# Optimization experiments

Hardware: AMD Instinct MI355X
Metric: run time of the kernel (lower is better)

The kernel has to match this reference:

```python
import jax, jax.numpy as jnp
import numpy as np

N, D_IN, H, C, K = 16384, 2048, 4096, 256, 256


def setup_inputs() -> dict:
    key = jax.random.key(0)
    ks = jax.random.split(key, 13)

    def lin(kw, kb, fan_in, fan_out):
        # torch Linear default init: U(-1/sqrt(fan_in), 1/sqrt(fan_in)); stored as [in, out]
        bound = 1.0 / np.sqrt(fan_in)
        W = jax.random.uniform(kw, (fan_in, fan_out), jnp.float32, -bound, bound)
        b = jax.random.uniform(kb, (fan_out,), jnp.float32, -bound, bound)
        return W, b

    W_e1, b_e1 = lin(ks[0], ks[1], D_IN, H)
    W_e2, b_e2 = lin(ks[2], ks[3], H, C)
    W_d1, b_d1 = lin(ks[4], ks[5], C, H)
    W_d2, b_d2 = lin(ks[6], ks[7], H, D_IN)
    # codebooks init U(-1/K, 1/K) per the torch code
    cb1 = jax.random.uniform(ks[8], (K, C), jnp.float32, -1.0 / K, 1.0 / K)
    cb2 = jax.random.uniform(ks[9], (K, C), jnp.float32, -1.0 / K, 1.0 / K)
    cb3 = jax.random.uniform(ks[10], (K, C), jnp.float32, -1.0 / K, 1.0 / K)
    x = jax.random.normal(ks[11], (N, D_IN), jnp.float32)
    return {"x": x, "W_e1": W_e1, "b_e1": b_e1, "W_e2": W_e2, "b_e2": b_e2,
            "cb1": cb1, "cb2": cb2, "cb3": cb3,
            "W_d1": W_d1, "b_d1": b_d1, "W_d2": W_d2, "b_d2": b_d2}


def _vq_stage(z, cb):
    # dist[n,k] = sum_c (cb[k,c] - z[n,c])^2 = ||z||^2 - 2 z.cb^T + ||cb||^2
    # (same math as the torch N x K x C broadcast, expressed as a GEMM)
    d = (jnp.sum(z * z, axis=1, keepdims=True)
         - 2.0 * (z @ cb.T)
         + jnp.sum(cb * cb, axis=1))            # [N, K]
    nearest = jnp.argmin(d, axis=1)             # [N]
    zq = cb[nearest]                            # gather [N, C]
    return nearest, zq


def reference(x, W_e1, b_e1, W_e2, b_e2, cb1, cb2, cb3, W_d1, b_d1, W_d2, b_d2):
    ze_1 = jax.nn.relu(x @ W_e1 + b_e1) @ W_e2 + b_e2     # [N, C]
    nearest_1, zq_1 = _vq_stage(ze_1, cb1)
    ze_2 = ze_1 - zq_1
    nearest_2, zq_2 = _vq_stage(ze_2, cb2)
    ze_3 = ze_2 - zq_2
    nearest_3, zq_3 = _vq_stage(ze_3, cb3)
    # straight-through estimator
    decoder_input = ze_1 + jax.lax.stop_gradient(zq_1 + zq_2 + zq_3 - ze_1)
    x_hat = jax.nn.sigmoid(decoder_input @ W_d1 + b_d1) @ W_d2 + b_d2
    return (x_hat, ze_1, ze_2, ze_3, zq_1, zq_2, zq_3, nearest_1, nearest_2, nearest_3)
```

## Files before the change

kernel.cpp:

```cpp
#include <hip/hip_runtime.h>
#include <cstddef>


#define NN 16384
#define DIN 2048
#define HH 4096
#define CC 256

typedef __attribute__((ext_vector_type(8))) short bf16x8;
typedef __attribute__((ext_vector_type(4))) float f32x4;

__device__ inline unsigned short f2b(float v) {
    unsigned int u = __float_as_uint(v);
    return (unsigned short)((u + 0x7fffu + ((u >> 16) & 1u)) >> 16);
}
__device__ inline float b2f(unsigned short s) {
    return __uint_as_float(((unsigned int)s) << 16);
}

template<int NP>
__launch_bounds__(256)
__global__ void tsplit(const float* __restrict__ W,
                       unsigned short* __restrict__ T0,
                       unsigned short* __restrict__ T1,
                       unsigned short* __restrict__ T2,
                       int K, int N)
{
    __shared__ float tile[32][33];
    const int k0 = blockIdx.y * 32, n0 = blockIdx.x * 32;
    const int c = threadIdx.x & 31, r = threadIdx.x >> 5;
    #pragma unroll
    for (int i = 0; i < 4; ++i)
        tile[r + 8*i][c] = W[(size_t)(k0 + r + 8*i) * N + n0 + c];
    __syncthreads();
    #pragma unroll
    for (int i = 0; i < 4; ++i) {
        const int nl = r + 8*i, kl = c;
        float v = tile[kl][nl];
        size_t o = (size_t)(n0 + nl) * K + k0 + kl;
        unsigned short h = f2b(v);
        T0[o] = h;
        if (NP > 1) {
            float r1 = v - b2f(h);
            unsigned short m = f2b(r1);
            T1[o] = m;
            T2[o] = f2b(r1 - b2f(m));
        }
    }
}

template<int NP, int EPI>
__launch_bounds__(256)
__global__ void gemm_sp(const float* __restrict__ A,
                        const unsigned short* __restrict__ B0,
                        const unsigned short* __restrict__ B1,
                        const unsigned short* __restrict__ B2,
                        const float* __restrict__ bias,
                        float* __restrict__ Cf,
                        int M, int N, int K)
{
    __shared__ unsigned short As[NP][128][32];
    __shared__ unsigned short Bs[NP][128][32];

    const int t    = threadIdx.x;
    const int wid  = t >> 6;
    const int lane = t & 63;
    const int bm   = blockIdx.y * 128;
    const int bn   = blockIdx.x * 128;
    const int wm   = (wid >> 1) * 64;
    const int wn   = (wid & 1) * 64;
    const int l15  = lane & 15;
    const int l4   = lane >> 4;

    f32x4 acc[4][4] = {};

    const unsigned short* Bp[3] = {B0, B1, B2};

    for (int k0 = 0; k0 < K; k0 += 32) {
        float4 av[4];
        #pragma unroll
        for (int i = 0; i < 4; ++i) {
            const int chunk = t + i * 256;
            const int arow  = chunk >> 3;
            const int ac4   = (chunk & 7) << 2;
            av[i] = *(const float4*)(A + (size_t)(bm + arow) * K + k0 + ac4);
        }
        bf16x8 bv[NP][2];
        #pragma unroll
        for (int p = 0; p < NP; ++p)
            #pragma unroll
            for (int i = 0; i < 2; ++i) {
                const int chunk = t + i * 256;
                const int brow  = chunk >> 2;
                const int bc8   = (chunk & 3) << 3;
                bv[p][i] = *(const bf16x8*)(Bp[p] + (size_t)(bn + brow) * K + k0 + bc8);
            }

        __syncthreads();

        #pragma unroll
        for (int i = 0; i < 4; ++i) {
            const int chunk = t + i * 256;
            const int arow  = chunk >> 3;
            const int ac4   = (chunk & 7) << 2;
            float vs[4] = {av[i].x, av[i].y, av[i].z, av[i].w};
            ushort4 hv, mv, lv;
            unsigned short* hp = (unsigned short*)&hv;
            unsigned short* mp = (unsigned short*)&mv;
            unsigned short* lp = (unsigned short*)&lv;
            #pragma unroll
            for (int j = 0; j < 4; ++j) {
                float v = vs[j];
                unsigned short h = f2b(v);
                hp[j] = h;
                if (NP > 1) {
                    float r1 = v - b2f(h);
                    unsigned short m = f2b(r1);
                    mp[j] = m;
                    lp[j] = f2b(r1 - b2f(m));
                }
            }
            *(ushort4*)&As[0][arow][ac4] = hv;
            if (NP > 1) {
                *(ushort4*)&As[1][arow][ac4] = mv;
                *(ushort4*)&As[2][arow][ac4] = lv;
            }
        }
        #pragma unroll
        for (int p = 0; p < NP; ++p)
            #pragma unroll
            for (int i = 0; i < 2; ++i) {
                const int chunk = t + i * 256;
                const int brow  = chunk >> 2;
                const int bc8   = (chunk & 3) << 3;
                *(bf16x8*)&Bs[p][brow][bc8] = bv[p][i];
            }

        __syncthreads();

        const int nprod = (NP == 3) ? 6 : 1;
        const int pa[6] = {0, 0, 1, 0, 1, 2};
        const int pb[6] = {0, 1, 0, 2, 1, 0};
        #pragma unroll
        for (int q = 0; q < 6; ++q) {
            if (q >= nprod) break;
            const int ia = pa[q], ib = pb[q];
            bf16x8 af[4], bfr[4];
            #pragma unroll
            for (int mi = 0; mi < 4; ++mi)
                af[mi] = *(const bf16x8*)&As[ia][wm + mi*16 + l15][l4 * 8];
            #pragma unroll
            for (int ni = 0; ni < 4; ++ni)
                bfr[ni] = *(const bf16x8*)&Bs[ib][wn + ni*16 + l15][l4 * 8];
            #pragma unroll
            for (int mi = 0; mi < 4; ++mi)
                #pragma unroll
                for (int ni = 0; ni < 4; ++ni)
                    acc[mi][ni] = __builtin_amdgcn_mfma_f32_16x16x32_bf16(
                        af[mi], bfr[ni], acc[mi][ni], 0, 0, 0);
        }
    }

    #pragma unroll
    for (int ni = 0; ni < 4; ++ni) {
        const int gcol = bn + wn + ni*16 + l15;
        const float bvv = bias[gcol];
        #pragma unroll
        for (int mi = 0; mi < 4; ++mi) {
            #pragma unroll
            for (int r = 0; r < 4; ++r) {
                float v = acc[mi][ni][r] + bvv;
                if (EPI == 1) v = fmaxf(v, 0.0f);
                if (EPI == 2) v = 1.0f / (1.0f + expf(-v));
                const int grow = bm + wm + mi*16 + l4*4 + r;
                Cf[(size_t)grow * N + gcol] = v;
            }
        }
    }
}

template<int EPI>
__launch_bounds__(256)
__global__ void gemm_f32(const float* __restrict__ A, const float* __restrict__ B,
                         const float* __restrict__ bias, float* __restrict__ C,
                         int M, int N, int K)
{
    __shared__ float As[16][132];
    __shared__ float Bs[16][132];
    const int t  = threadIdx.x;
    const int tx = t & 15;
    const int ty = t >> 4;
    const int bm = blockIdx.y * 128;
    const int bn = blockIdx.x * 128;
    const int ar  = t >> 2;
    const int ac  = (t & 3) << 2;
    const int bkr = t >> 5;
    const int bc  = (t & 31) << 2;
    const float* Ap0 = A + (size_t)(bm + ar)      * K + ac;
    const float* Ap1 = A + (size_t)(bm + ar + 64) * K + ac;
    const float* Bp0 = B + (size_t)bkr       * N + bn + bc;
    const float* Bp1 = B + (size_t)(bkr + 8) * N + bn + bc;
    float acc[8][8] = {};
    for (int k0 = 0; k0 < K; k0 += 16) {
        float4 a0 = *(const float4*)(Ap0 + k0);
        float4 a1 = *(const float4*)(Ap1 + k0);
        float4 b0 = *(const float4*)(Bp0 + (size_t)k0 * N);
        float4 b1 = *(const float4*)(Bp1 + (size_t)k0 * N);
        __syncthreads();
        As[ac+0][ar] = a0.x; As[ac+1][ar] = a0.y;
        As[ac+2][ar] = a0.z; As[ac+3][ar] = a0.w;
        As[ac+0][ar+64] = a1.x; As[ac+1][ar+64] = a1.y;
        As[ac+2][ar+64] = a1.z; As[ac+3][ar+64] = a1.w;
        *(float4*)&Bs[bkr][bc]   = b0;
        *(float4*)&Bs[bkr+8][bc] = b1;
        __syncthreads();
        #pragma unroll
        for (int k = 0; k < 16; ++k) {
            float4 xa0 = *(const float4*)&As[k][ty*8];
            float4 xa1 = *(const float4*)&As[k][ty*8+4];
            float4 xb0 = *(const float4*)&Bs[k][tx*8];
            float4 xb1 = *(const float4*)&Bs[k][tx*8+4];
            float avr[8] = {xa0.x,xa0.y,xa0.z,xa0.w,xa1.x,xa1.y,xa1.z,xa1.w};
            float bvr[8] = {xb0.x,xb0.y,xb0.z,xb0.w,xb1.x,xb1.y,xb1.z,xb1.w};
            #pragma unroll
            for (int i = 0; i < 8; ++i)
                #pragma unroll
                for (int j = 0; j < 8; ++j)
                    acc[i][j] = fmaf(avr[i], bvr[j], acc[i][j]);
        }
    }
    float4 bb0 = *(const float4*)(bias + bn + tx*8);
    float4 bb1 = *(const float4*)(bias + bn + tx*8 + 4);
    float bcol[8] = {bb0.x,bb0.y,bb0.z,bb0.w,bb1.x,bb1.y,bb1.z,bb1.w};
    #pragma unroll
    for (int i = 0; i < 8; ++i) {
        const int row = bm + ty*8 + i;
        float o[8];
        #pragma unroll
        for (int j = 0; j < 8; ++j) {
            float v = acc[i][j] + bcol[j];
            if (EPI == 1) v = fmaxf(v, 0.0f);
            if (EPI == 2) v = 1.0f / (1.0f + expf(-v));
            o[j] = v;
        }
        float4 o0 = {o[0],o[1],o[2],o[3]};
        float4 o1 = {o[4],o[5],o[6],o[7]};
        float* cp = C + (size_t)row * N + bn + tx*8;
        *(float4*)cp       = o0;
        *(float4*)(cp + 4) = o1;
    }
}

__launch_bounds__(256)
__global__ void vq_kernel(const float* __restrict__ ze1,
                          const float* __restrict__ cb1,
                          const float* __restrict__ cb2,
                          const float* __restrict__ cb3,
                          float* __restrict__ out_ze2, float* __restrict__ out_ze3,
                          float* __restrict__ out_zq1, float* __restrict__ out_zq2,
                          float* __restrict__ out_zq3,
                          float* __restrict__ out_n1,  float* __restrict__ out_n2,
                          float* __restrict__ out_n3,
                          float* __restrict__ dec_in)
{
    __shared__ float Zs[16][260];
    __shared__ float Ds[16][260];
    __shared__ float DecS[16][260];
    __shared__ float Srow[16];
    __shared__ int   Kmin[16];

    const int t    = threadIdx.x;
    const int row0 = blockIdx.x * 16;

    for (int i = t; i < 16*64; i += 256) {
        int r = i >> 6, c4 = (i & 63) << 2;
        float4 v = *(const float4*)(ze1 + (size_t)(row0 + r) * 256 + c4);
        *(float4*)&Zs[r][c4] = v;
        float4 z = {0.f,0.f,0.f,0.f};
        *(float4*)&DecS[r][c4] = z;
    }
    __syncthreads();

    const float* cbs[3] = {cb1, cb2, cb3};
    float* zqs[3] = {out_zq1, out_zq2, out_zq3};
    float* nss[3] = {out_n1, out_n2, out_n3};

    for (int s = 0; s < 3; ++s) {
        const float* cb = cbs[s];
        if (t < 16) {
            float ssum = 0.f;
            for (int c = 0; c < 256; ++c) ssum = fmaf(Zs[t][c], Zs[t][c], ssum);
            Srow[t] = ssum;
        }
        __syncthreads();
        {
            float accr[16];
            #pragma unroll
            for (int r = 0; r < 16; ++r) accr[r] = 0.f;
            float c2 = 0.f;
            const float* cbrow = cb + (size_t)t * 256;
            for (int c4 = 0; c4 < 256; c4 += 4) {
                float4 cv = *(const float4*)(cbrow + c4);
                c2 = fmaf(cv.x,cv.x,fmaf(cv.y,cv.y,fmaf(cv.z,cv.z,fmaf(cv.w,cv.w,c2))));
                #pragma unroll
                for (int r = 0; r < 16; ++r) {
                    float4 zv = *(const float4*)&Zs[r][c4];
                    accr[r] = fmaf(zv.x,cv.x,fmaf(zv.y,cv.y,
                              fmaf(zv.z,cv.z,fmaf(zv.w,cv.w,accr[r]))));
                }
            }
            #pragma unroll
            for (int r = 0; r < 16; ++r) {
                float g2 = __fmul_rn(2.0f, accr[r]);
                float t1 = __fsub_rn(Srow[r], g2);
                Ds[r][t]  = __fadd_rn(t1, c2);
            }
        }
        __syncthreads();
        if (t < 16) {
            float best = Ds[t][0];
            int bk = 0;
            for (int k = 1; k < 256; ++k) {
                float v = Ds[t][k];
                if (v < best) { best = v; bk = k; }
            }
            Kmin[t] = bk;
            nss[s][row0 + t] = (float)bk;
        }
        __syncthreads();
        for (int i = t; i < 16*64; i += 256) {
            int r = i >> 6, c4 = (i & 63) << 2;
            const float* q = cb + (size_t)Kmin[r] * 256 + c4;
            float4 qv = *(const float4*)q;
            *(float4*)&zqs[s][(size_t)(row0 + r) * 256 + c4] = qv;
            float4 dv = *(float4*)&DecS[r][c4];
            dv.x = __fadd_rn(dv.x, qv.x); dv.y = __fadd_rn(dv.y, qv.y);
            dv.z = __fadd_rn(dv.z, qv.z); dv.w = __fadd_rn(dv.w, qv.w);
            *(float4*)&DecS[r][c4] = dv;
            if (s < 2) {
                float4 zv = *(float4*)&Zs[r][c4];
                zv.x = __fsub_rn(zv.x, qv.x); zv.y = __fsub_rn(zv.y, qv.y);
                zv.z = __fsub_rn(zv.z, qv.z); zv.w = __fsub_rn(zv.w, qv.w);
                *(float4*)&Zs[r][c4] = zv;
                float* oz = (s == 0) ? out_ze2 : out_ze3;
                *(float4*)&oz[(size_t)(row0 + r) * 256 + c4] = zv;
            }
        }
        __syncthreads();
    }

    for (int i = t; i < 16*64; i += 256) {
        int r = i >> 6, c4 = (i & 63) << 2;
        float4 z1 = *(const float4*)(ze1 + (size_t)(row0 + r) * 256 + c4);
        float4 dv = *(float4*)&DecS[r][c4];
        float4 o;
        o.x = __fadd_rn(z1.x, __fsub_rn(dv.x, z1.x));
        o.y = __fadd_rn(z1.y, __fsub_rn(dv.y, z1.y));
        o.z = __fadd_rn(z1.z, __fsub_rn(dv.z, z1.z));
        o.w = __fadd_rn(z1.w, __fsub_rn(dv.w, z1.w));
        *(float4*)&dec_in[(size_t)(row0 + r) * 256 + c4] = o;
    }
}

extern "C" void kernel_launch(void* const* d_in, const int* in_sizes, int n_in,
                              void* d_out, int out_size, void* d_ws, size_t ws_size,
                              hipStream_t stream)
{
    const float* x   = (const float*)d_in[0];
    const float* We1 = (const float*)d_in[1];
    const float* be1 = (const float*)d_in[2];
    const float* We2 = (const float*)d_in[3];
    const float* be2 = (const float*)d_in[4];
    const float* cb1 = (const float*)d_in[5];
    const float* cb2 = (const float*)d_in[6];
    const float* cb3 = (const float*)d_in[7];
    const float* Wd1 = (const float*)d_in[8];
    const float* bd1 = (const float*)d_in[9];
    const float* Wd2 = (const float*)d_in[10];
    const float* bd2 = (const float*)d_in[11];

    float* out   = (float*)d_out;
    float* x_hat = out;
    float* ze1   = out + 33554432;
    float* ze2   = out + 37748736;
    float* ze3   = out + 41943040;
    float* zq1   = out + 46137344;
    float* zq2   = out + 50331648;
    float* zq3   = out + 54525952;
    float* n1    = out + 58720256;
    float* n2    = out + 58736640;
    float* n3    = out + 58753024;

    float* h   = (float*)d_ws;
    float* dec = h + (size_t)NN * HH;
    unsigned short* We1t = (unsigned short*)(dec + (size_t)NN * CC);
    size_t szWe1 = (size_t)HH * DIN;
    unsigned short* We2t = We1t + 3 * szWe1;
    size_t szWe2 = (size_t)CC * HH;
    unsigned short* Wd1t = We2t + 3 * szWe2;
    size_t szWd1 = (size_t)HH * CC;
    unsigned short* Wd2t = Wd1t + szWd1;
    size_t szWd2 = (size_t)DIN * HH;
    size_t need = (size_t)((unsigned short*)(Wd2t + szWd2) - (unsigned short*)d_ws) * 2;

    dim3 blk(256);

    if (ws_size >= need) {
        tsplit<3><<<dim3(HH/32, DIN/32), blk, 0, stream>>>(We1, We1t, We1t+szWe1, We1t+2*szWe1, DIN, HH);
        tsplit<3><<<dim3(CC/32, HH/32),  blk, 0, stream>>>(We2, We2t, We2t+szWe2, We2t+2*szWe2, HH, CC);
        tsplit<1><<<dim3(HH/32, CC/32),  blk, 0, stream>>>(Wd1, Wd1t, nullptr, nullptr, CC, HH);
        tsplit<1><<<dim3(DIN/32, HH/32), blk, 0, stream>>>(Wd2, Wd2t, nullptr, nullptr, HH, DIN);

        gemm_sp<3,1><<<dim3(HH/128, NN/128), blk, 0, stream>>>(x, We1t, We1t+szWe1, We1t+2*szWe1, be1, h, NN, HH, DIN);
        gemm_sp<3,0><<<dim3(CC/128, NN/128), blk, 0, stream>>>(h, We2t, We2t+szWe2, We2t+2*szWe2, be2, ze1, NN, CC, HH);
        vq_kernel<<<dim3(NN/16), blk, 0, stream>>>(ze1, cb1, cb2, cb3,
                                                   ze2, ze3, zq1, zq2, zq3,
                                                   n1, n2, n3, dec);
        gemm_sp<1,2><<<dim3(HH/128, NN/128), blk, 0, stream>>>(dec, Wd1t, nullptr, nullptr, bd1, h, NN, HH, CC);
        gemm_sp<1,0><<<dim3(DIN/128, NN/128), blk, 0, stream>>>(h, Wd2t, nullptr, nullptr, bd2, x_hat, NN, DIN, HH);
    } else {
        float* h1  = (float*)d_ws;
        float* dcf = h1 + (size_t)NN * HH;
        gemm_f32<1><<<dim3(HH/128, NN/128), blk, 0, stream>>>(x, We1, be1, h1, NN, HH, DIN);
        gemm_f32<0><<<dim3(CC/128, NN/128), blk, 0, stream>>>(h1, We2, be2, ze1, NN, CC, HH);
        vq_kernel<<<dim3(NN/16), blk, 0, stream>>>(ze1, cb1, cb2, cb3,
                                                   ze2, ze3, zq1, zq2, zq3,
                                                   n1, n2, n3, dcf);
        gemm_f32<2><<<dim3(HH/128, NN/128), blk, 0, stream>>>(dcf, Wd1, bd1, h1, NN, HH, CC);
        gemm_f32<0><<<dim3(DIN/128, NN/128), blk, 0, stream>>>(h1, Wd2, bd2, x_hat, NN, DIN, HH);
    }
}
```

Baseline: 2.538 ms.

## Pre-split activations to bf16 planes, load tiles via global_load_lds with swizzle

Activations are now split into three bf16 planes ahead of time, either by a dedicated kernel or in the previous GEMM's epilogue, so the GEMMs stream pre-split A tiles straight into LDS with global_load_lds. The LDS layout is XOR-swizzled and workgroup IDs are remapped for L2 locality. The decoder path now stores intermediates as single bf16 instead of fp32, which halves activation traffic. The goal is to cut per-tile split arithmetic, register staging and LDS bank conflicts. The cost is much more workspace and memory writes for the 3-plane hidden activations.

```diff
diff --git a/kernel.cpp b/kernel.cpp
--- a/kernel.cpp
+++ b/kernel.cpp
@@ -7,23 +7,37 @@
 #define HH 4096
 #define CC 256
 
+typedef unsigned short ushortT;
 typedef __attribute__((ext_vector_type(8))) short bf16x8;
 typedef __attribute__((ext_vector_type(4))) float f32x4;
 
-__device__ inline unsigned short f2b(float v) {
+__device__ __forceinline__ ushortT f2b(float v) {
     unsigned int u = __float_as_uint(v);
-    return (unsigned short)((u + 0x7fffu + ((u >> 16) & 1u)) >> 16);
-}
-__device__ inline float b2f(unsigned short s) {
+    return (ushortT)((u + 0x7fffu + ((u >> 16) & 1u)) >> 16);
+}
+__device__ __forceinline__ float b2f(ushortT s) {
     return __uint_as_float(((unsigned int)s) << 16);
+}
+__device__ __forceinline__ void split3(float v, ushortT& h, ushortT& m, ushortT& l) {
+    h = f2b(v);
+    float r1 = v - b2f(h);
+    m = f2b(r1);
+    l = f2b(r1 - b2f(m));
+}
+
+__device__ __forceinline__ void gld16(const void* g, void* l) {
+    __builtin_amdgcn_global_load_lds(
+        (const __attribute__((address_space(1))) unsigned int*)g,
+        (__attribute__((address_space(3))) unsigned int*)l,
+        16, 0, 0);
 }
 
 template<int NP>
 __launch_bounds__(256)
 __global__ void tsplit(const float* __restrict__ W,
-                       unsigned short* __restrict__ T0,
-                       unsigned short* __restrict__ T1,
-                       unsigned short* __restrict__ T2,
+                       ushortT* __restrict__ T0,
+                       ushortT* __restrict__ T1,
+                       ushortT* __restrict__ T2,
                        int K, int N)
 {
     __shared__ float tile[32][33];
@@ -38,126 +52,173 @@
         const int nl = r + 8*i, kl = c;
         float v = tile[kl][nl];
         size_t o = (size_t)(n0 + nl) * K + k0 + kl;
-        unsigned short h = f2b(v);
+        ushortT h = f2b(v);
         T0[o] = h;
         if (NP > 1) {
             float r1 = v - b2f(h);
-            unsigned short m = f2b(r1);
+            ushortT m = f2b(r1);
             T1[o] = m;
             T2[o] = f2b(r1 - b2f(m));
         }
     }
 }
 
-template<int NP, int EPI>
 __launch_bounds__(256)
-__global__ void gemm_sp(const float* __restrict__ A,
-                        const unsigned short* __restrict__ B0,
-                        const unsigned short* __restrict__ B1,
-                        const unsigned short* __restrict__ B2,
+__global__ void split_src(const float* __restrict__ X,
+                          ushortT* __restrict__ P0, ushortT* __restrict__ P1,
+                          ushortT* __restrict__ P2, size_t n4)
+{
+    for (size_t i = (size_t)blockIdx.x * 256 + threadIdx.x; i < n4;
+         i += (size_t)gridDim.x * 256) {
+        float4 v = *(const float4*)(X + i * 4);
+        ushort4 hv, mv, lv;
+        split3(v.x, ((ushortT*)&hv)[0], ((ushortT*)&mv)[0], ((ushortT*)&lv)[0]);
+        split3(v.y, ((ushortT*)&hv)[1], ((ushortT*)&mv)[1], ((ushortT*)&lv)[1]);
+        split3(v.z, ((ushortT*)&hv)[2], ((ushortT*)&mv)[2], ((ushortT*)&lv)[2]);
+        split3(v.w, ((ushortT*)&hv)[3], ((ushortT*)&mv)[3], ((ushortT*)&lv)[3]);
+        *(ushort4*)(P0 + i * 4) = hv;
+        *(ushort4*)(P1 + i * 4) = mv;
+        *(ushort4*)(P2 + i * 4) = lv;
+    }
+}
+
+template<int NPA, int INA, int EPI, int OM>
+__launch_bounds__(256)
+__global__ void gemm_mp(const float* __restrict__ Af,
+                        const ushortT* __restrict__ Ap0,
+                        const ushortT* __restrict__ Ap1,
+                        const ushortT* __restrict__ Ap2,
+                        const ushortT* __restrict__ B0,
+                        const ushortT* __restrict__ B1,
+                        const ushortT* __restrict__ B2,
                         const float* __restrict__ bias,
                         float* __restrict__ Cf,
+                        ushortT* __restrict__ O0, ushortT* __restrict__ O1,
+                        ushortT* __restrict__ O2,
                         int M, int N, int K)
 {
-    __shared__ unsigned short As[NP][128][32];
-    __shared__ unsigned short Bs[NP][128][32];
+    __shared__ ushortT sh[2 * NPA * 4096];
 
     const int t    = threadIdx.x;
     const int wid  = t >> 6;
     const int lane = t & 63;
-    const int bm   = blockIdx.y * 128;
-    const int bn   = blockIdx.x * 128;
-    const int wm   = (wid >> 1) * 64;
-    const int wn   = (wid & 1) * 64;
     const int l15  = lane & 15;
     const int l4   = lane >> 4;
 
+    const int gx  = gridDim.x;
+    const int nwg = gx * gridDim.y;
+    const int lin = blockIdx.y * gx + blockIdx.x;
+    const int swz = (lin & 7) * (nwg >> 3) + (lin >> 3);
+    const int bm  = (swz / gx) * 128;
+    const int bn  = (swz % gx) * 128;
+
+    const int wm = (wid >> 1) * 64;
+    const int wn = (wid & 1) * 64;
+
+    const ushortT* APs[3] = {Ap0, Ap1, Ap2};
+    const ushortT* BPs[3] = {B0, B1, B2};
+
+    const int CHB = 2 * NPA;
+    const int CHA = (INA == 1) ? 2 * NPA : 0;
+    const ushortT* gpA[(INA == 1) ? 2 * NPA : 1];
+    const ushortT* gpB[2 * NPA];
+    if (INA == 1) {
+        #pragma unroll
+        for (int i = 0; i < CHA; ++i) {
+            int chunk = i * 256 + t;
+            int plane = chunk >> 9;
+            int c     = chunk & 511;
+            int row   = c >> 2;
+            int colsw = (c & 3) ^ ((c >> 4) & 3);
+            gpA[i] = APs[plane] + (size_t)(bm + row) * K + colsw * 8;
+        }
+    }
+    #pragma unroll
+    for (int i = 0; i < CHB; ++i) {
+        int chunk = i * 256 + t;
+        int plane = chunk >> 9;
+        int c     = chunk & 511;
+        int row   = c >> 2;
+        int colsw = (c & 3) ^ ((c >> 4) & 3);
+        gpB[i] = BPs[plane] + (size_t)(bn + row) * K + colsw * 8;
+    }
+    const int arow_ = t >> 3;
+    const int ac4_  = (t & 7) << 2;
+    const int aswc_ = ((ac4_ >> 3) ^ ((arow_ >> 2) & 3)) * 8 + (ac4_ & 7);
+
+    const int sws = (l4 ^ (l15 >> 2)) * 8;
+
     f32x4 acc[4][4] = {};
-
-    const unsigned short* Bp[3] = {B0, B1, B2};
 
     for (int k0 = 0; k0 < K; k0 += 32) {
         float4 av[4];
+        if (INA == 0) {
+            #pragma unroll
+            for (int i = 0; i < 4; ++i) {
+                const int chunk = t + i * 256;
+                const int arow  = chunk >> 3;
+                const int ac4   = (chunk & 7) << 2;
+                av[i] = *(const float4*)(Af + (size_t)(bm + arow) * K + k0 + ac4);
+            }
+        }
+
+        __syncthreads();
+
+        if (INA == 1) {
+            #pragma unroll
+            for (int i = 0; i < CHA; ++i) {
+                gld16(gpA[i], sh + ((size_t)i * 256 + t) * 8);
+                gpA[i] += 32;
+            }
+        }
         #pragma unroll
-        for (int i = 0; i < 4; ++i) {
-            const int chunk = t + i * 256;
-            const int arow  = chunk >> 3;
-            const int ac4   = (chunk & 7) << 2;
-            av[i] = *(const float4*)(A + (size_t)(bm + arow) * K + k0 + ac4);
-        }
-        bf16x8 bv[NP][2];
+        for (int i = 0; i < CHB; ++i) {
+            gld16(gpB[i], sh + (size_t)NPA * 4096 + ((size_t)i * 256 + t) * 8);
+            gpB[i] += 32;
+        }
+        if (INA == 0) {
+            #pragma unroll
+            for (int i = 0; i < 4; ++i) {
+                const int chunk = t + i * 256;
+                const int arow  = chunk >> 3;
+                const int ac4   = (chunk & 7) << 2;
+                const int swc   = ((ac4 >> 3) ^ ((arow >> 2) & 3)) * 8 + (ac4 & 7);
+                float vs[4] = {av[i].x, av[i].y, av[i].z, av[i].w};
+                ushort4 hv, mv, lv;
+                #pragma unroll
+                for (int j = 0; j < 4; ++j)
+                    split3(vs[j], ((ushortT*)&hv)[j], ((ushortT*)&mv)[j],
+                           ((ushortT*)&lv)[j]);
+                *(ushort4*)&sh[0 * 4096 + arow * 32 + swc] = hv;
+                if (NPA > 1) {
+                    *(ushort4*)&sh[1 * 4096 + arow * 32 + swc] = mv;
+                    *(ushort4*)&sh[2 * 4096 + arow * 32 + swc] = lv;
+                }
+            }
+        }
+
+        __syncthreads();
+
         #pragma unroll
-        for (int p = 0; p < NP; ++p)
-            #pragma unroll
-            for (int i = 0; i < 2; ++i) {
-                const int chunk = t + i * 256;
-                const int brow  = chunk >> 2;
-                const int bc8   = (chunk & 3) << 3;
-                bv[p][i] = *(const bf16x8*)(Bp[p] + (size_t)(bn + brow) * K + k0 + bc8);
-            }
-
-        __syncthreads();
-
-        #pragma unroll
-        for (int i = 0; i < 4; ++i) {
-            const int chunk = t + i * 256;
-            const int arow  = chunk >> 3;
-            const int ac4   = (chunk & 7) << 2;
-            float vs[4] = {av[i].x, av[i].y, av[i].z, av[i].w};
-            ushort4 hv, mv, lv;
-            unsigned short* hp = (unsigned short*)&hv;
-            unsigned short* mp = (unsigned short*)&mv;
-            unsigned short* lp = (unsigned short*)&lv;
-            #pragma unroll
-            for (int j = 0; j < 4; ++j) {
-                float v = vs[j];
-                unsigned short h = f2b(v);
-                hp[j] = h;
-                if (NP > 1) {
-                    float r1 = v - b2f(h);
-                    unsigned short m = f2b(r1);
-                    mp[j] = m;
-                    lp[j] = f2b(r1 - b2f(m));
-                }
-            }
-            *(ushort4*)&As[0][arow][ac4] = hv;
-            if (NP > 1) {
-                *(ushort4*)&As[1][arow][ac4] = mv;
-                *(ushort4*)&As[2][arow][ac4] = lv;
-            }
-        }
-        #pragma unroll
-        for (int p = 0; p < NP; ++p)
-            #pragma unroll
-            for (int i = 0; i < 2; ++i) {
-                const int chunk = t + i * 256;
-                const int brow  = chunk >> 2;
-                const int bc8   = (chunk & 3) << 3;
-                *(bf16x8*)&Bs[p][brow][bc8] = bv[p][i];
-            }
-
-        __syncthreads();
-
-        const int nprod = (NP == 3) ? 6 : 1;
-        const int pa[6] = {0, 0, 1, 0, 1, 2};
-        const int pb[6] = {0, 1, 0, 2, 1, 0};
-        #pragma unroll
-        for (int q = 0; q < 6; ++q) {
-            if (q >= nprod) break;
-            const int ia = pa[q], ib = pb[q];
-            bf16x8 af[4], bfr[4];
+        for (int pa = 0; pa < NPA; ++pa) {
+            bf16x8 af[4];
             #pragma unroll
             for (int mi = 0; mi < 4; ++mi)
-                af[mi] = *(const bf16x8*)&As[ia][wm + mi*16 + l15][l4 * 8];
-            #pragma unroll
-            for (int ni = 0; ni < 4; ++ni)
-                bfr[ni] = *(const bf16x8*)&Bs[ib][wn + ni*16 + l15][l4 * 8];
-            #pragma unroll
-            for (int mi = 0; mi < 4; ++mi)
+                af[mi] = *(const bf16x8*)&sh[pa * 4096 + (wm + mi*16 + l15) * 32 + sws];
+            #pragma unroll
+            for (int pb = 0; pb < NPA - pa; ++pb) {
+                bf16x8 bfr[4];
                 #pragma unroll
                 for (int ni = 0; ni < 4; ++ni)
-                    acc[mi][ni] = __builtin_amdgcn_mfma_f32_16x16x32_bf16(
-                        af[mi], bfr[ni], acc[mi][ni], 0, 0, 0);
+                    bfr[ni] = *(const bf16x8*)&sh[(NPA + pb) * 4096 +
+                                                  (wn + ni*16 + l15) * 32 + sws];
+                #pragma unroll
+                for (int mi = 0; mi < 4; ++mi)
+                    #pragma unroll
+                    for (int ni = 0; ni < 4; ++ni)
+                        acc[mi][ni] = __builtin_amdgcn_mfma_f32_16x16x32_bf16(
+                            af[mi], bfr[ni], acc[mi][ni], 0, 0, 0);
+            }
         }
     }
 
@@ -173,81 +234,18 @@
                 if (EPI == 1) v = fmaxf(v, 0.0f);
                 if (EPI == 2) v = 1.0f / (1.0f + expf(-v));
                 const int grow = bm + wm + mi*16 + l4*4 + r;
-                Cf[(size_t)grow * N + gcol] = v;
-            }
-        }
-    }
-}
-
-template<int EPI>
-__launch_bounds__(256)
-__global__ void gemm_f32(const float* __restrict__ A, const float* __restrict__ B,
-                         const float* __restrict__ bias, float* __restrict__ C,
-                         int M, int N, int K)
-{
-    __shared__ float As[16][132];
-    __shared__ float Bs[16][132];
-    const int t  = threadIdx.x;
-    const int tx = t & 15;
-    const int ty = t >> 4;
-    const int bm = blockIdx.y * 128;
-    const int bn = blockIdx.x * 128;
-    const int ar  = t >> 2;
-    const int ac  = (t & 3) << 2;
-    const int bkr = t >> 5;
-    const int bc  = (t & 31) << 2;
-    const float* Ap0 = A + (size_t)(bm + ar)      * K + ac;
-    const float* Ap1 = A + (size_t)(bm + ar + 64) * K + ac;
-    const float* Bp0 = B + (size_t)bkr       * N + bn + bc;
-    const float* Bp1 = B + (size_t)(bkr + 8) * N + bn + bc;
-    float acc[8][8] = {};
-    for (int k0 = 0; k0 < K; k0 += 16) {
-        float4 a0 = *(const float4*)(Ap0 + k0);
-        float4 a1 = *(const float4*)(Ap1 + k0);
-        float4 b0 = *(const float4*)(Bp0 + (size_t)k0 * N);
-        float4 b1 = *(const float4*)(Bp1 + (size_t)k0 * N);
-        __syncthreads();
-        As[ac+0][ar] = a0.x; As[ac+1][ar] = a0.y;
-        As[ac+2][ar] = a0.z; As[ac+3][ar] = a0.w;
-        As[ac+0][ar+64] = a1.x; As[ac+1][ar+64] = a1.y;
-        As[ac+2][ar+64] = a1.z; As[ac+3][ar+64] = a1.w;
-        *(float4*)&Bs[bkr][bc]   = b0;
-        *(float4*)&Bs[bkr+8][bc] = b1;
-        __syncthreads();
-        #pragma unroll
-        for (int k = 0; k < 16; ++k) {
-            float4 xa0 = *(const float4*)&As[k][ty*8];
-            float4 xa1 = *(const float4*)&As[k][ty*8+4];
-            float4 xb0 = *(const float4*)&Bs[k][tx*8];
-            float4 xb1 = *(const float4*)&Bs[k][tx*8+4];
-            float avr[8] = {xa0.x,xa0.y,xa0.z,xa0.w,xa1.x,xa1.y,xa1.z,xa1.w};
-            float bvr[8] = {xb0.x,xb0.y,xb0.z,xb0.w,xb1.x,xb1.y,xb1.z,xb1.w};
-            #pragma unroll
-            for (int i = 0; i < 8; ++i)
-                #pragma unroll
-                for (int j = 0; j < 8; ++j)
-                    acc[i][j] = fmaf(avr[i], bvr[j], acc[i][j]);
-        }
-    }
-    float4 bb0 = *(const float4*)(bias + bn + tx*8);
-    float4 bb1 = *(const float4*)(bias + bn + tx*8 + 4);
-    float bcol[8] = {bb0.x,bb0.y,bb0.z,bb0.w,bb1.x,bb1.y,bb1.z,bb1.w};
-    #pragma unroll
-    for (int i = 0; i < 8; ++i) {
-        const int row = bm + ty*8 + i;
-        float o[8];
-        #pragma unroll
-        for (int j = 0; j < 8; ++j) {
-            float v = acc[i][j] + bcol[j];
-            if (EPI == 1) v = fmaxf(v, 0.0f);
-            if (EPI == 2) v = 1.0f / (1.0f + expf(-v));
-            o[j] = v;
-        }
-        float4 o0 = {o[0],o[1],o[2],o[3]};
-        float4 o1 = {o[4],o[5],o[6],o[7]};
-        float* cp = C + (size_t)row * N + bn + tx*8;
-        *(float4*)cp       = o0;
-        *(float4*)(cp + 4) = o1;
+                const size_t o = (size_t)grow * N + gcol;
+                if (OM == 0) {
+                    Cf[o] = v;
+                } else if (OM == 2) {
+                    O0[o] = f2b(v);
+                } else {
+                    ushortT hh, mm, ll;
+                    split3(v, hh, mm, ll);
+                    O0[o] = hh; O1[o] = mm; O2[o] = ll;
+                }
+            }
+        }
     }
 }
 
@@ -261,7 +259,7 @@
                           float* __restrict__ out_zq3,
                           float* __restrict__ out_n1,  float* __restrict__ out_n2,
                           float* __restrict__ out_n3,
-                          float* __restrict__ dec_in)
+                          ushortT* __restrict__ dec_p)
 {
     __shared__ float Zs[16][260];
     __shared__ float Ds[16][260];
@@ -358,7 +356,12 @@
         o.y = __fadd_rn(z1.y, __fsub_rn(dv.y, z1.y));
         o.z = __fadd_rn(z1.z, __fsub_rn(dv.z, z1.z));
         o.w = __fadd_rn(z1.w, __fsub_rn(dv.w, z1.w));
-        *(float4*)&dec_in[(size_t)(row0 + r) * 256 + c4] = o;
+        ushort4 ov;
+        ((ushortT*)&ov)[0] = f2b(o.x);
+        ((ushortT*)&ov)[1] = f2b(o.y);
+        ((ushortT*)&ov)[2] = f2b(o.z);
+        ((ushortT*)&ov)[3] = f2b(o.w);
+        *(ushort4*)(dec_p + (size_t)(row0 + r) * 256 + c4) = ov;
     }
 }
 
@@ -391,42 +394,79 @@
     float* n2    = out + 58736640;
     float* n3    = out + 58753024;
 
-    float* h   = (float*)d_ws;
-    float* dec = h + (size_t)NN * HH;
-    unsigned short* We1t = (unsigned short*)(dec + (size_t)NN * CC);
-    size_t szWe1 = (size_t)HH * DIN;
-    unsigned short* We2t = We1t + 3 * szWe1;
-    size_t szWe2 = (size_t)CC * HH;
-    unsigned short* Wd1t = We2t + 3 * szWe2;
-    size_t szWd1 = (size_t)HH * CC;
-    unsigned short* Wd2t = Wd1t + szWd1;
-    size_t szWd2 = (size_t)DIN * HH;
-    size_t need = (size_t)((unsigned short*)(Wd2t + szWd2) - (unsigned short*)d_ws) * 2;
+    const size_t szX  = (size_t)NN * DIN;
+    const size_t szH  = (size_t)NN * HH;
+    const size_t szD  = (size_t)NN * CC;
+    const size_t szW1 = (size_t)HH * DIN;
+    const size_t szW2 = (size_t)CC * HH;
+
+    const size_t needA = (3*szX + 3*szH + 3*szW1 + 3*szW2 + szW2 + szW1) * 2;
 
     dim3 blk(256);
 
-    if (ws_size >= need) {
-        tsplit<3><<<dim3(HH/32, DIN/32), blk, 0, stream>>>(We1, We1t, We1t+szWe1, We1t+2*szWe1, DIN, HH);
-        tsplit<3><<<dim3(CC/32, HH/32),  blk, 0, stream>>>(We2, We2t, We2t+szWe2, We2t+2*szWe2, HH, CC);
+    if (ws_size >= needA) {
+        ushortT* xp0 = (ushortT*)d_ws;
+        ushortT* xp1 = xp0 + szX;
+        ushortT* xp2 = xp1 + szX;
+        ushortT* hp0 = xp2 + szX;
+        ushortT* hp1 = hp0 + szH;
+        ushortT* hp2 = hp1 + szH;
+        ushortT* We1t = hp2 + szH;
+        ushortT* We2t = We1t + 3*szW1;
+        ushortT* Wd1t = We2t + 3*szW2;
+        ushortT* Wd2t = Wd1t + szW2;
+        ushortT* decp = xp0;
+        ushortT* h2p  = xp0 + szD;
+
+        tsplit<3><<<dim3(HH/32, DIN/32), blk, 0, stream>>>(We1, We1t, We1t+szW1, We1t+2*szW1, DIN, HH);
+        tsplit<3><<<dim3(CC/32, HH/32),  blk, 0, stream>>>(We2, We2t, We2t+szW2, We2t+2*szW2, HH, CC);
         tsplit<1><<<dim3(HH/32, CC/32),  blk, 0, stream>>>(Wd1, Wd1t, nullptr, nullptr, CC, HH);
         tsplit<1><<<dim3(DIN/32, HH/32), blk, 0, stream>>>(Wd2, Wd2t, nullptr, nullptr, HH, DIN);
-
-        gemm_sp<3,1><<<dim3(HH/128, NN/128), blk, 0, stream>>>(x, We1t, We1t+szWe1, We1t+2*szWe1, be1, h, NN, HH, DIN);
-        gemm_sp<3,0><<<dim3(CC/128, NN/128), blk, 0, stream>>>(h, We2t, We2t+szWe2, We2t+2*szWe2, be2, ze1, NN, CC, HH);
+        split_src<<<dim3(4096), blk, 0, stream>>>(x, xp0, xp1, xp2, szX/4);
+
+        gemm_mp<3,1,1,1><<<dim3(HH/128, NN/128), blk, 0, stream>>>(
+            nullptr, xp0, xp1, xp2, We1t, We1t+szW1, We1t+2*szW1, be1,
+            nullptr, hp0, hp1, hp2, NN, HH, DIN);
+        gemm_mp<3,1,0,0><<<dim3(CC/128, NN/128), blk, 0, stream>>>(
+            nullptr, hp0, hp1, hp2, We2t, We2t+szW2, We2t+2*szW2, be2,
+            ze1, nullptr, nullptr, nullptr, NN, CC, HH);
         vq_kernel<<<dim3(NN/16), blk, 0, stream>>>(ze1, cb1, cb2, cb3,
                                                    ze2, ze3, zq1, zq2, zq3,
-                                                   n1, n2, n3, dec);
-        gemm_sp<1,2><<<dim3(HH/128, NN/128), blk, 0, stream>>>(dec, Wd1t, nullptr, nullptr, bd1, h, NN, HH, CC);
-        gemm_sp<1,0><<<dim3(DIN/128, NN/128), blk, 0, stream>>>(h, Wd2t, nullptr, nullptr, bd2, x_hat, NN, DIN, HH);
+                                                   n1, n2, n3, decp);
+        gemm_mp<1,1,2,2><<<dim3(HH/128, NN/128), blk, 0, stream>>>(
+            nullptr, decp, nullptr, nullptr, Wd1t, nullptr, nullptr, bd1,
+            nullptr, h2p, nullptr, nullptr, NN, HH, CC);
+        gemm_mp<1,1,0,0><<<dim3(DIN/128, NN/128), blk, 0, stream>>>(
+            nullptr, h2p, nullptr, nullptr, Wd2t, nullptr, nullptr, bd2,
+            x_hat, nullptr, nullptr, nullptr, NN, DIN, HH);
     } else {
-        float* h1  = (float*)d_ws;
-        float* dcf = h1 + (size_t)NN * HH;
-        gemm_f32<1><<<dim3(HH/128, NN/128), blk, 0, stream>>>(x, We1, be1, h1, NN, HH, DIN);
-        gemm_f32<0><<<dim3(CC/128, NN/128), blk, 0, stream>>>(h1, We2, be2, ze1, NN, CC, HH);
+        float* hf = (float*)d_ws;
+        ushortT* decp = (ushortT*)(hf + szH);
+        ushortT* We1t = decp + szD;
+        ushortT* We2t = We1t + 3*szW1;
+        ushortT* Wd1t = We2t + 3*szW2;
+        ushortT* Wd2t = Wd1t + szW2;
+        ushortT* h2p  = (ushortT*)hf;
+
+        tsplit<3><<<dim3(HH/32, DIN/32), blk, 0, stream>>>(We1, We1t, We1t+szW1, We1t+2*szW1, DIN, HH);
+        tsplit<3><<<dim3(CC/32, HH/32),  blk, 0, stream>>>(We2, We2t, We2t+szW2, We2t+2*szW2, HH, CC);
+        tsplit<1><<<dim3(HH/32, CC/32),  blk, 0, stream>>>(Wd1, Wd1t, nullptr, nullptr, CC, HH);
+        tsplit<1><<<dim3(DIN/32, HH/32), blk, 0, stream>>>(Wd2, Wd2t, nullptr, nullptr, HH, DIN);
+
+        gemm_mp<3,0,1,0><<<dim3(HH/128, NN/128), blk, 0, stream>>>(
+            x, nullptr, nullptr, nullptr, We1t, We1t+szW1, We1t+2*szW1, be1,
+            hf, nullptr, nullptr, nullptr, NN, HH, DIN);
+        gemm_mp<3,0,0,0><<<dim3(CC/128, NN/128), blk, 0, stream>>>(
+            hf, nullptr, nullptr, nullptr, We2t, We2t+szW2, We2t+2*szW2, be2,
+            ze1, nullptr, nullptr, nullptr, NN, CC, HH);
         vq_kernel<<<dim3(NN/16), blk, 0, stream>>>(ze1, cb1, cb2, cb3,
                                                    ze2, ze3, zq1, zq2, zq3,
-                                                   n1, n2, n3, dcf);
-        gemm_f32<2><<<dim3(HH/128, NN/128), blk, 0, stream>>>(dcf, Wd1, bd1, h1, NN, HH, CC);
-        gemm_f32<0><<<dim3(DIN/128, NN/128), blk, 0, stream>>>(h1, Wd2, bd2, x_hat, NN, DIN, HH);
-    }
-}
+                                                   n1, n2, n3, decp);
+        gemm_mp<1,1,2,2><<<dim3(HH/128, NN/128), blk, 0, stream>>>(
+            nullptr, decp, nullptr, nullptr, Wd1t, nullptr, nullptr, bd1,
+            nullptr, h2p, nullptr, nullptr, NN, HH, CC);
+        gemm_mp<1,1,0,0><<<dim3(DIN/128, NN/128), blk, 0, stream>>>(
+            nullptr, h2p, nullptr, nullptr, Wd2t, nullptr, nullptr, bd2,
+            x_hat, nullptr, nullptr, nullptr, NN, DIN, HH);
+    }
+}
```

After: 3.499 ms. 37.9% more time.
